# Kernel tuning notes

Hardware: AMD Instinct MI355X
Metric: run time of the kernel (lower is better)

Reference implementation:

```python
import jax, jax.numpy as jnp
import numpy as np

P = 4; PSIZE = 16; EPS = 1e-8; LAM = 1e-3; MF = 2.0; ITERS = 2
BATCH = 64; A = 64; B = 8; C = 16; D = 16; E = 10


def _conv2d(x, w, b, stride, pad):
    y = jax.lax.conv_general_dilated(x, w, (stride, stride), [(pad, pad), (pad, pad)],
                                     dimension_numbers=('NCHW', 'OIHW', 'NCHW'))
    return y + b[None, :, None, None]


def _patches(x, K, stride):
    # x: (b, H, W, F) -> (b, oh, ow, K, K, F) sliding KxK windows with given stride
    b, H, W, F = x.shape
    oh = (H - K) // stride + 1
    ow = (W - K) // stride + 1
    ih = jnp.arange(oh) * stride
    iw = jnp.arange(ow) * stride
    p = x[:, ih[:, None] + jnp.arange(K)[None, :]]          # (b, oh, K, W, F)
    p = p[:, :, :, iw[:, None] + jnp.arange(K)[None, :]]    # (b, oh, K, ow, K, F)
    return p.transpose(0, 1, 3, 2, 4, 5), oh, ow


def _fuzzy_routing(v, a_in, beta_u, beta_a):
    # Fuzzy (c-means style) routing. v: (n, N, Cout, PSIZE) votes, a_in: (n, N).
    n, N, Cc, _ = v.shape
    r = jnp.full((n, N, Cc), 1.0 / Cc, dtype=v.dtype)
    aw = a_in[:, :, None]
    for t in range(ITERS):
        rm = (r ** MF) * aw                                             # fuzzified, activation-weighted
        coeff = rm / (jnp.sum(rm, axis=1, keepdims=True) + EPS)         # (n, N, C)
        mu = jnp.einsum('bnc,bncp->bcp', coeff, v)                      # (n, C, PSIZE)
        if t < ITERS - 1:
            dist = jnp.sum((v - mu[:, None]) ** 2, axis=-1) + EPS       # (n, N, C)
            inv = dist ** (-1.0 / (MF - 1.0))
            r = inv / (jnp.sum(inv, axis=2, keepdims=True) + EPS)
    sigma_sq = jnp.einsum('bnc,bncp->bcp', coeff, (v - mu[:, None]) ** 2) + EPS
    r_sum = jnp.sum((r ** MF) * aw, axis=1)                             # (n, C)
    cost = (beta_u[None, :, None] + 0.5 * jnp.log(sigma_sq)) * r_sum[:, :, None]
    a_out = jax.nn.sigmoid(LAM * (beta_a[None, :] - jnp.sum(cost, axis=2)))
    return mu, a_out


def _conv_caps(pose, a, W, beta_u, beta_a, K, stride):
    # pose: (b, H, W, Bi, PSIZE), a: (b, H, W, Bi); W: (K*K*Bi, Co, P, P)
    b, H, Wd, Bi, _ = pose.shape
    Co = W.shape[1]
    pp, oh, ow = _patches(pose.reshape(b, H, Wd, Bi * PSIZE), K, stride)
    ap, _, _ = _patches(a, K, stride)
    n = b * oh * ow
    pp = pp.reshape(n, K * K * Bi, P, P)
    ap = ap.reshape(n, K * K * Bi)
    v = jnp.einsum('nipq,icqr->nicpr', pp, W).reshape(n, K * K * Bi, Co, PSIZE)
    mu, a_out = _fuzzy_routing(v, ap, beta_u, beta_a)
    return mu.reshape(b, oh, ow, Co, PSIZE), a_out.reshape(b, oh, ow, Co)


def _class_caps(pose, a, W, beta_u, beta_a):
    # K=1, weight-shared over positions, with coordinate addition.
    b, H, Wd, Bi, _ = pose.shape
    Co = W.shape[1]
    v = jnp.einsum('bhwipq,icqr->bhwicpr', pose.reshape(b, H, Wd, Bi, P, P), W)
    v = v.reshape(b, H, Wd, Bi, Co, PSIZE)
    ch = (jnp.arange(H, dtype=v.dtype) / H)[None, :, None, None, None]
    cw = (jnp.arange(Wd, dtype=v.dtype) / Wd)[None, None, :, None, None]
    v = v.at[..., 0].add(ch)
    v = v.at[..., 1].add(cw)
    v = v.reshape(b, H * Wd * Bi, Co, PSIZE)
    return _fuzzy_routing(v, a.reshape(b, -1), beta_u, beta_a)


def setup_inputs():
    key = jax.random.key(0)
    ks = jax.random.split(key, 8)
    return {
        'x': jax.random.normal(ks[0], (BATCH, 1, 32, 32), jnp.float32),
        'conv1_w': jax.random.normal(ks[1], (A, 1, 5, 5), jnp.float32) * 0.1,
        'conv1_b': jnp.zeros((A,), jnp.float32),
        'bn_g': jnp.ones((A,), jnp.float32),
        'bn_b': jnp.zeros((A,), jnp.float32),
        'bn_mean': jnp.zeros((A,), jnp.float32),
        'bn_var': jnp.ones((A,), jnp.float32),
        'prim_pose_w': jax.random.normal(ks[2], (B * PSIZE, A, 1, 1), jnp.float32) * 0.1,
        'prim_pose_b': jnp.zeros((B * PSIZE,), jnp.float32),
        'prim_a_w': jax.random.normal(ks[3], (B, A, 1, 1), jnp.float32) * 0.1,
        'prim_a_b': jnp.zeros((B,), jnp.float32),
        'w1': jax.random.normal(ks[4], (3 * 3 * B, C, P, P), jnp.float32),
        'bu1': jnp.zeros((C,), jnp.float32),
        'ba1': jnp.zeros((C,), jnp.float32),
        'w2': jax.random.normal(ks[5], (3 * 3 * C, D, P, P), jnp.float32),
        'bu2': jnp.zeros((D,), jnp.float32),
        'ba2': jnp.zeros((D,), jnp.float32),
        'wc': jax.random.normal(ks[6], (D, E, P, P), jnp.float32),
        'buc': jnp.zeros((E,), jnp.float32),
        'bac': jnp.zeros((E,), jnp.float32),
    }


def reference(x, conv1_w, conv1_b, bn_g, bn_b, bn_mean, bn_var,
              prim_pose_w, prim_pose_b, prim_a_w, prim_a_b,
              w1, bu1, ba1, w2, bu2, ba2, wc, buc, bac):
    y = _conv2d(x, conv1_w, conv1_b, 2, 2)                               # (b, A, 16, 16)
    inv_std = jax.lax.rsqrt(bn_var + 1e-3)
    y = (y - bn_mean[None, :, None, None]) * (bn_g * inv_std)[None, :, None, None] + bn_b[None, :, None, None]
    y = jax.nn.relu(y)
    pose = _conv2d(y, prim_pose_w, prim_pose_b, 1, 0)                    # (b, B*16, 16, 16)
    a = jax.nn.sigmoid(_conv2d(y, prim_a_w, prim_a_b, 1, 0))             # (b, B, 16, 16)
    b_, _, H, Wd = a.shape
    pose = pose.transpose(0, 2, 3, 1).reshape(b_, H, Wd, B, PSIZE)
    a = a.transpose(0, 2, 3, 1)
    pose1, a1 = _conv_caps(pose, a, w1, bu1, ba1, 3, 2)
    pose2, a2 = _conv_caps(pose1, a1, w2, bu2, ba2, 3, 1)
    _, a_class = _class_caps(pose2, a2, wc, buc, bac)                    # (b, E)
    return a_class
```

## Files before the change

kernel.cpp:

```cpp
#include <hip/hip_runtime.h>
#include <math.h>

#define EPS_ 1e-8f
#define LAM_ 1e-3f

__global__ __launch_bounds__(256) void k_conv_bn(
    const float* __restrict__ x, const float* __restrict__ cw, const float* __restrict__ cb,
    const float* __restrict__ g, const float* __restrict__ bb,
    const float* __restrict__ mean, const float* __restrict__ var,
    float* __restrict__ y)
{
    int t = blockIdx.x * 256 + threadIdx.x;
    int ch = t & 63, w = (t >> 6) & 15, h = (t >> 10) & 15, b = t >> 14;
    const float* xb = x + b * 1024;
    const float* wc = cw + ch * 25;
    float acc = cb[ch];
    #pragma unroll
    for (int kh = 0; kh < 5; ++kh) {
        int ih = h * 2 - 2 + kh;
        if (ih < 0 || ih > 31) continue;
        #pragma unroll
        for (int kw = 0; kw < 5; ++kw) {
            int iw = w * 2 - 2 + kw;
            if (iw < 0 || iw > 31) continue;
            acc = fmaf(xb[ih * 32 + iw], wc[kh * 5 + kw], acc);
        }
    }
    float v = (acc - mean[ch]) * (g[ch] * rsqrtf(var[ch] + 1e-3f)) + bb[ch];
    y[t] = fmaxf(v, 0.f);
}

__global__ __launch_bounds__(256) void k_transw(
    const float* __restrict__ w1, const float* __restrict__ w2, const float* __restrict__ wc,
    const float* __restrict__ pw, const float* __restrict__ pb,
    const float* __restrict__ aw, const float* __restrict__ ab,
    float* __restrict__ w1t, float* __restrict__ w2t, float* __restrict__ wct,
    float* __restrict__ wpt)
{
    int t = blockIdx.x * 256 + threadIdx.x;
    if (t < 3616 * 16) {
        int m = t >> 4, e = t & 15, r = e >> 2, q = e & 3;
        const float* src; float* dst;
        if (m < 1152)      { src = w1 + m * 16;          dst = w1t + m * 16; }
        else if (m < 3456) { src = w2 + (m - 1152) * 16; dst = w2t + (m - 1152) * 16; }
        else               { src = wc + (m - 3456) * 16; dst = wct + (m - 3456) * 16; }
        dst[e] = src[q * 4 + r];
    } else if (t < 3616 * 16 + 65 * 136) {
        int idx = t - 3616 * 16;
        int o = idx % 136, j = idx / 136;
        float v;
        if (j == 64)       v = (o < 128) ? pb[o] : ab[o - 128];
        else if (o < 128)  v = pw[o * 64 + j];
        else               v = aw[(o - 128) * 64 + j];
        wpt[j * 136 + o] = v;
    }
}

__global__ __launch_bounds__(256) void k_prim(
    const float* __restrict__ y, const float* __restrict__ wpt,
    float* __restrict__ poseP, float* __restrict__ aP)
{
    int t = blockIdx.x * 256 + threadIdx.x;
    if (t >= 16384 * 34) return;
    int oq = t % 34;
    int pos = t / 34;
    const float* yp = y + pos * 64;
    float4 acc = *(const float4*)(wpt + 64 * 136 + oq * 4);
    #pragma unroll
    for (int j0 = 0; j0 < 64; j0 += 4) {
        float4 y4 = *(const float4*)(yp + j0);
        float4 w0 = *(const float4*)(wpt + (j0 + 0) * 136 + oq * 4);
        float4 w1 = *(const float4*)(wpt + (j0 + 1) * 136 + oq * 4);
        float4 w2 = *(const float4*)(wpt + (j0 + 2) * 136 + oq * 4);
        float4 w3 = *(const float4*)(wpt + (j0 + 3) * 136 + oq * 4);
        acc.x = fmaf(y4.x, w0.x, fmaf(y4.y, w1.x, fmaf(y4.z, w2.x, fmaf(y4.w, w3.x, acc.x))));
        acc.y = fmaf(y4.x, w0.y, fmaf(y4.y, w1.y, fmaf(y4.z, w2.y, fmaf(y4.w, w3.y, acc.y))));
        acc.z = fmaf(y4.x, w0.z, fmaf(y4.y, w1.z, fmaf(y4.z, w2.z, fmaf(y4.w, w3.z, acc.z))));
        acc.w = fmaf(y4.x, w0.w, fmaf(y4.y, w1.w, fmaf(y4.z, w2.w, fmaf(y4.w, w3.w, acc.w))));
    }
    if (oq < 32) {
        ((float4*)(poseP + pos * 128))[oq] = acc;
    } else {
        int oo = (oq - 32) * 4;
        float* ad = aP + pos * 8 + oo;
        ad[0] = 1.f / (1.f + __expf(-acc.x));
        ad[1] = 1.f / (1.f + __expf(-acc.y));
        ad[2] = 1.f / (1.f + __expf(-acc.z));
        ad[3] = 1.f / (1.f + __expf(-acc.w));
    }
}

template<int N, int C, int K, int S, int H, int W, int Bi, int OH, int OW, int NW>
__global__ __launch_bounds__(NW * 64) void k_caps_split(
    const float* __restrict__ pose_in,
    const float* __restrict__ a_in,
    const float* __restrict__ Wt,
    const float* __restrict__ bu, const float* __restrict__ ba,
    float* __restrict__ pose_out,
    float* __restrict__ a_out)
{
    static_assert(C == 16 && N % (NW * 4) == 0, "");
    constexpr int BLK = NW * 64;
    constexpr int IW  = N / NW;
    constexpr int NIT = IW / 4;

    __shared__ __align__(16) float pp[N * 16];
    __shared__ float ap[N];
    __shared__ __align__(16) float red1[NW][16][20];
    __shared__ __align__(16) float red2[NW][16][20];
    __shared__ float redr[NW][16];

    const int t = threadIdx.x;
    const int w = t >> 6, lane = t & 63;
    const int n_ = blockIdx.x;
    const int b = n_ / (OH * OW);
    const int rem = n_ % (OH * OW);
    const int oh = rem / OW, ow = rem % OW;

    for (int idx = t; idx < N * 4; idx += BLK) {
        int i = idx >> 2, f = idx & 3;
        int bi = i % Bi;
        int k2 = i / Bi;
        int sw = ow * S + (k2 % K), sh = oh * S + (k2 / K);
        const float4* src = (const float4*)(pose_in + (((b * H + sh) * W + sw) * Bi + bi) * 16);
        ((float4*)(pp + i * 16))[f] = src[f];
    }
    for (int i = t; i < N; i += BLK) {
        int bi = i % Bi;
        int k2 = i / Bi;
        int sw = ow * S + (k2 % K), sh = oh * S + (k2 / K);
        ap[i] = a_in[((b * H + sh) * W + sw) * Bi + bi];
    }
    __syncthreads();

    float suma = 0.f;
    for (int i = lane; i < N; i += 64) suma += ap[i];
    #pragma unroll
    for (int m = 1; m < 64; m <<= 1) suma += __shfl_xor(suma, m, 64);
    const float inv0 = __builtin_amdgcn_rcpf(suma + (float)(C * C) * EPS_);

    const int ig = (lane >> 4) & 3, cc = lane & 15;
    const int ibase = w * IW;

    float muU[16];
    #pragma unroll
    for (int e2 = 0; e2 < 16; ++e2) muU[e2] = 0.f;
    #pragma unroll 2
    for (int ii = 0; ii < NIT; ++ii) {
        int i = ibase + ig + ii * 4;
        const float4* pi4 = (const float4*)(pp + i * 16);
        const float4* wt4 = (const float4*)(Wt + (i * C + cc) * 16);
        float4 pv[4] = { pi4[0], pi4[1], pi4[2], pi4[3] };
        float4 wv[4] = { wt4[0], wt4[1], wt4[2], wt4[3] };
        float co = ap[i] * inv0;
        #pragma unroll
        for (int e2 = 0; e2 < 16; ++e2) {
            float4 p4 = pv[e2 >> 2], w4 = wv[e2 & 3];
            float v = p4.x * w4.x + p4.y * w4.y + p4.z * w4.z + p4.w * w4.w;
            muU[e2] = fmaf(co, v, muU[e2]);
        }
    }
    #pragma unroll
    for (int e2 = 0; e2 < 16; ++e2) {
        muU[e2] += __shfl_xor(muU[e2], 16, 64);
        muU[e2] += __shfl_xor(muU[e2], 32, 64);
    }
    if (lane < 16) {
        float4* dst = (float4*)&red1[w][lane][0];
        dst[0] = *(float4*)&muU[0];
        dst[1] = *(float4*)&muU[4];
        dst[2] = *(float4*)&muU[8];
        dst[3] = *(float4*)&muU[12];
    }
    __syncthreads();

    float m0[16];
    {
        #pragma unroll
        for (int f = 0; f < 4; ++f) {
            float4 s = *(const float4*)&red1[0][cc][f * 4];
            #pragma unroll
            for (int ww = 1; ww < NW; ++ww) {
                float4 p = *(const float4*)&red1[ww][cc][f * 4];
                s.x += p.x; s.y += p.y; s.z += p.z; s.w += p.w;
            }
            *(float4*)&m0[f * 4] = s;
        }
    }
    __syncthreads();

    float SvU[16], Sv2U[16];
    #pragma unroll
    for (int e2 = 0; e2 < 16; ++e2) { SvU[e2] = 0.f; Sv2U[e2] = 0.f; }
    float rsum = 0.f;
    #pragma unroll 2
    for (int ii = 0; ii < NIT; ++ii) {
        int i = ibase + ig + ii * 4;
        const float4* pi4 = (const float4*)(pp + i * 16);
        const float4* wt4 = (const float4*)(Wt + (i * C + cc) * 16);
        float4 pv[4] = { pi4[0], pi4[1], pi4[2], pi4[3] };
        float4 wv[4] = { wt4[0], wt4[1], wt4[2], wt4[3] };
        float vv[16];
        float dist = EPS_;
        #pragma unroll
        for (int e2 = 0; e2 < 16; ++e2) {
            float4 p4 = pv[e2 >> 2], w4 = wv[e2 & 3];
            float v = p4.x * w4.x + p4.y * w4.y + p4.z * w4.z + p4.w * w4.w;
            vv[e2] = v;
            float d = v - m0[e2];
            dist = fmaf(d, d, dist);
        }
        float inv = __builtin_amdgcn_rcpf(dist);
        float s = inv;
        #pragma unroll
        for (int m = 1; m < 16; m <<= 1) s += __shfl_xor(s, m, 64);
        float r1 = inv * __builtin_amdgcn_rcpf(s + EPS_);
        float rm = r1 * r1 * ap[i];
        rsum += rm;
        #pragma unroll
        for (int e2 = 0; e2 < 16; ++e2) {
            float rv = rm * vv[e2];
            SvU[e2] += rv;
            Sv2U[e2] = fmaf(rv, vv[e2], Sv2U[e2]);
        }
    }
    #pragma unroll
    for (int e2 = 0; e2 < 16; ++e2) {
        SvU[e2] += __shfl_xor(SvU[e2], 16, 64);
        SvU[e2] += __shfl_xor(SvU[e2], 32, 64);
        Sv2U[e2] += __shfl_xor(Sv2U[e2], 16, 64);
        Sv2U[e2] += __shfl_xor(Sv2U[e2], 32, 64);
    }
    rsum += __shfl_xor(rsum, 16, 64);
    rsum += __shfl_xor(rsum, 32, 64);
    if (lane < 16) {
        float4* d1 = (float4*)&red1[w][lane][0];
        float4* d2 = (float4*)&red2[w][lane][0];
        d1[0] = *(float4*)&SvU[0];  d1[1] = *(float4*)&SvU[4];
        d1[2] = *(float4*)&SvU[8];  d1[3] = *(float4*)&SvU[12];
        d2[0] = *(float4*)&Sv2U[0]; d2[1] = *(float4*)&Sv2U[4];
        d2[2] = *(float4*)&Sv2U[8]; d2[3] = *(float4*)&Sv2U[12];
        redr[w][lane] = rsum;
    }
    __syncthreads();

    if (w == 0) {
        float SvT[16], Sv2T[16];
        #pragma unroll
        for (int f = 0; f < 4; ++f) {
            float4 s1 = *(const float4*)&red1[0][cc][f * 4];
            float4 s2 = *(const float4*)&red2[0][cc][f * 4];
            #pragma unroll
            for (int ww = 1; ww < NW; ++ww) {
                float4 p1 = *(const float4*)&red1[ww][cc][f * 4];
                float4 p2 = *(const float4*)&red2[ww][cc][f * 4];
                s1.x += p1.x; s1.y += p1.y; s1.z += p1.z; s1.w += p1.w;
                s2.x += p2.x; s2.y += p2.y; s2.z += p2.z; s2.w += p2.w;
            }
            *(float4*)&SvT[f * 4] = s1;
            *(float4*)&Sv2T[f * 4] = s2;
        }
        float R = 0.f;
        #pragma unroll
        for (int ww = 0; ww < NW; ++ww) R += redr[ww][cc];

        const float id = 1.f / (R + EPS_);
        const float S0 = R * id;
        const float buc_ = bu[cc];
        float cs = 0.f;
        float4 outv[4];
        #pragma unroll
        for (int e2 = 0; e2 < 16; ++e2) {
            float Sv = SvT[e2] * id;
            float Sv2 = Sv2T[e2] * id;
            float sigma = fmaxf(Sv2 + Sv * Sv * (S0 - 2.f), 0.f) + EPS_;
            cs += (buc_ + 0.5f * __logf(sigma)) * R;
            ((float*)outv)[e2] = Sv;
        }
        if (lane < 16) {
            float4* pd = (float4*)(pose_out + (n_ * C + cc) * 16);
            pd[0] = outv[0]; pd[1] = outv[1]; pd[2] = outv[2]; pd[3] = outv[3];
            a_out[n_ * C + cc] = 1.f / (1.f + __expf(-(LAM_ * (ba[cc] - cs))));
        }
    }
}

template<int N, int C, int H, int W, int Bi, int BLK>
__global__ __launch_bounds__(BLK) void k_caps_class(
    const float* __restrict__ pose_in, const float* __restrict__ a_in,
    const float* __restrict__ Wt,
    const float* __restrict__ bu, const float* __restrict__ ba,
    float* __restrict__ a_out)
{
    constexpr int NW  = BLK / 64;
    constexpr int NIG = BLK / 16;
    constexpr int NIT = (N + NIG - 1) / NIG;

    __shared__ __align__(16) float pp[N * 16];
    __shared__ float ap[N];
    __shared__ float coeff0[N];
    __shared__ float mu0[16 * 17];
    __shared__ float red1[NW * C * 17];
    __shared__ float red2[NW * C * 17];
    __shared__ float redr[NW * C];

    const int t = threadIdx.x;
    const int lane = t & 63;
    const int w = t >> 6;
    const int b = blockIdx.x;

    for (int idx = t; idx < N * 4; idx += BLK) {
        int i = idx >> 2, f = idx & 3;
        int bi = i % Bi;
        int hw = i / Bi;
        int sw = hw % W, sh = hw / W;
        const float4* src = (const float4*)(pose_in + (((b * H + sh) * W + sw) * Bi + bi) * 16);
        ((float4*)(pp + i * 16))[f] = src[f];
    }
    for (int i = t; i < N; i += BLK) {
        int bi = i % Bi;
        int hw = i / Bi;
        int sw = hw % W, sh = hw / W;
        ap[i] = a_in[((b * H + sh) * W + sw) * Bi + bi];
    }
    __syncthreads();

    {
        float part = 0.f;
        for (int i = t; i < N; i += BLK) part += ap[i];
        #pragma unroll
        for (int m = 1; m < 64; m <<= 1) part += __shfl_xor(part, m, 64);
        if (lane == 0) red1[w] = part;
        __syncthreads();
        float s = 0.f;
        #pragma unroll
        for (int ww = 0; ww < NW; ++ww) s += red1[ww];
        float inv0 = __builtin_amdgcn_rcpf(s + (float)(C * C) * EPS_);
        for (int i = t; i < N; i += BLK) coeff0[i] = ap[i] * inv0;
        __syncthreads();
    }

    const int ig = t >> 4, cc = t & 15;

    {
        float muU[16];
        #pragma unroll
        for (int e2 = 0; e2 < 16; ++e2) muU[e2] = 0.f;
        if (cc < C) {
            for (int ii = 0; ii < NIT; ++ii) {
                int i = ig + ii * NIG;
                if (i < N) {
                    const float4* pi4 = (const float4*)(pp + i * 16);
                    const float4* wt4 = (const float4*)(Wt + ((i % Bi) * C + cc) * 16);
                    float4 pv[4] = { pi4[0], pi4[1], pi4[2], pi4[3] };
                    float4 wv[4] = { wt4[0], wt4[1], wt4[2], wt4[3] };
                    float co = coeff0[i];
                    float chv = (float)(i / (W * Bi)) * (1.f / H);
                    float cwv = (float)((i / Bi) % W) * (1.f / W);
                    #pragma unroll
                    for (int e2 = 0; e2 < 16; ++e2) {
                        float4 p4 = pv[e2 >> 2], w4 = wv[e2 & 3];
                        float v = p4.x * w4.x + p4.y * w4.y + p4.z * w4.z + p4.w * w4.w;
                        if (e2 == 0) v += chv;
                        if (e2 == 1) v += cwv;
                        muU[e2] = fmaf(co, v, muU[e2]);
                    }
                }
            }
        }
        #pragma unroll
        for (int e2 = 0; e2 < 16; ++e2) {
            float xv = muU[e2];
            xv += __shfl_xor(xv, 16, 64);
            xv += __shfl_xor(xv, 32, 64);
            if (lane < 16 && lane < C) red1[(w * C + lane) * 17 + e2] = xv;
        }
        __syncthreads();
        if (t < 256) {
            int c = t >> 4, e = t & 15;
            if (c < C) {
                float m = 0.f;
                #pragma unroll
                for (int ww = 0; ww < NW; ++ww) m += red1[(ww * C + c) * 17 + e];
                mu0[c * 17 + e] = m;
            }
        }
        __syncthreads();
    }

    {
        float m0[16];
        if (cc < C) {
            #pragma unroll
            for (int e2 = 0; e2 < 16; ++e2) m0[e2] = mu0[cc * 17 + e2];
        }
        float SvU[16], Sv2U[16];
        #pragma unroll
        for (int e2 = 0; e2 < 16; ++e2) { SvU[e2] = 0.f; Sv2U[e2] = 0.f; }
        float rsumP = 0.f;

        for (int ii = 0; ii < NIT; ++ii) {
            int i = ig + ii * NIG;
            bool act = (i < N);
            float inv = 0.f;
            float vv[16];
            if (act && cc < C) {
                const float4* pi4 = (const float4*)(pp + i * 16);
                const float4* wt4 = (const float4*)(Wt + ((i % Bi) * C + cc) * 16);
                float4 pv[4] = { pi4[0], pi4[1], pi4[2], pi4[3] };
                float4 wv[4] = { wt4[0], wt4[1], wt4[2], wt4[3] };
                float chv = (float)(i / (W * Bi)) * (1.f / H);
                float cwv = (float)((i / Bi) % W) * (1.f / W);
                float dist = EPS_;
                #pragma unroll
                for (int e2 = 0; e2 < 16; ++e2) {
                    float4 p4 = pv[e2 >> 2], w4 = wv[e2 & 3];
                    float v = p4.x * w4.x + p4.y * w4.y + p4.z * w4.z + p4.w * w4.w;
                    if (e2 == 0) v += chv;
                    if (e2 == 1) v += cwv;
                    vv[e2] = v;
                    float d = v - m0[e2];
                    dist = fmaf(d, d, dist);
                }
                inv = __builtin_amdgcn_rcpf(dist);
            }
            float s = inv;
            #pragma unroll
            for (int m = 1; m < 16; m <<= 1) s += __shfl_xor(s, m, 64);
            if (act && cc < C) {
                float r1 = inv * __builtin_amdgcn_rcpf(s + EPS_);
                float rm = r1 * r1 * ap[i];
                rsumP += rm;
                #pragma unroll
                for (int e2 = 0; e2 < 16; ++e2) {
                    SvU[e2] = fmaf(rm, vv[e2], SvU[e2]);
                    Sv2U[e2] = fmaf(rm * vv[e2], vv[e2], Sv2U[e2]);
                }
            }
        }
        #pragma unroll
        for (int e2 = 0; e2 < 16; ++e2) {
            float xv = SvU[e2];
            xv += __shfl_xor(xv, 16, 64);
            xv += __shfl_xor(xv, 32, 64);
            float yv = Sv2U[e2];
            yv += __shfl_xor(yv, 16, 64);
            yv += __shfl_xor(yv, 32, 64);
            if (lane < 16 && lane < C) {
                red1[(w * C + lane) * 17 + e2] = xv;
                red2[(w * C + lane) * 17 + e2] = yv;
            }
        }
        {
            float rv = rsumP;
            rv += __shfl_xor(rv, 16, 64);
            rv += __shfl_xor(rv, 32, 64);
            if (lane < 16 && lane < C) redr[w * C + lane] = rv;
        }
        __syncthreads();
    }

    if (t < 256) {
        int c = t >> 4, e = t & 15;
        if (c < C) {
            float SvT = 0.f, Sv2T = 0.f, R = 0.f;
            #pragma unroll
            for (int ww = 0; ww < NW; ++ww) {
                SvT  += red1[(ww * C + c) * 17 + e];
                Sv2T += red2[(ww * C + c) * 17 + e];
                R    += redr[ww * C + c];
            }
            float id = 1.f / (R + EPS_);
            float S0 = R * id;
            float Sv = SvT * id;
            float Sv2 = Sv2T * id;
            float sigma = fmaxf(Sv2 + Sv * Sv * (S0 - 2.f), 0.f) + EPS_;
            float cost = (bu[c] + 0.5f * __logf(sigma)) * R;
            float cs = cost;
            #pragma unroll
            for (int m = 1; m < 16; m <<= 1) cs += __shfl_xor(cs, m, 64);
            if (e == 0) a_out[b * C + c] = 1.f / (1.f + __expf(-(LAM_ * (ba[c] - cs))));
        }
    }
}

extern "C" void kernel_launch(void* const* d_in, const int* in_sizes, int n_in,
                              void* d_out, int out_size, void* d_ws, size_t ws_size,
                              hipStream_t stream)
{
    const float* x   = (const float*)d_in[0];
    const float* c1w = (const float*)d_in[1];
    const float* c1b = (const float*)d_in[2];
    const float* bng = (const float*)d_in[3];
    const float* bnb = (const float*)d_in[4];
    const float* bnm = (const float*)d_in[5];
    const float* bnv = (const float*)d_in[6];
    const float* ppw = (const float*)d_in[7];
    const float* ppb = (const float*)d_in[8];
    const float* paw = (const float*)d_in[9];
    const float* pab = (const float*)d_in[10];
    const float* w1  = (const float*)d_in[11];
    const float* bu1 = (const float*)d_in[12];
    const float* ba1 = (const float*)d_in[13];
    const float* w2  = (const float*)d_in[14];
    const float* bu2 = (const float*)d_in[15];
    const float* ba2 = (const float*)d_in[16];
    const float* wcp = (const float*)d_in[17];
    const float* buc = (const float*)d_in[18];
    const float* bac = (const float*)d_in[19];
    float* out = (float*)d_out;

    float* ws    = (float*)d_ws;
    float* y     = ws;
    float* poseP = y + 1048576;
    float* aP    = poseP + 2097152;
    float* pose1 = aP + 131072;
    float* a1    = pose1 + 802816;
    float* pose2 = a1 + 50176;
    float* a2    = pose2 + 409600;
    float* w1t   = a2 + 25600;
    float* w2t   = w1t + 18432;
    float* wct   = w2t + 36864;
    float* wpt   = wct + 2560;

    hipLaunchKernelGGL(k_transw, dim3((3616 * 16 + 65 * 136 + 255) / 256), dim3(256), 0, stream,
                       w1, w2, wcp, ppw, ppb, paw, pab, w1t, w2t, wct, wpt);
    hipLaunchKernelGGL(k_conv_bn, dim3(4096), dim3(256), 0, stream,
                       x, c1w, c1b, bng, bnb, bnm, bnv, y);
    hipLaunchKernelGGL(k_prim, dim3((16384 * 34 + 255) / 256), dim3(256), 0, stream,
                       y, wpt, poseP, aP);
    hipLaunchKernelGGL((k_caps_split<72, 16, 3, 2, 16, 16, 8, 7, 7, 2>), dim3(3136), dim3(128), 0, stream,
                       poseP, aP, w1t, bu1, ba1, pose1, a1);
    hipLaunchKernelGGL((k_caps_split<144, 16, 3, 1, 7, 7, 16, 5, 5, 4>), dim3(1600), dim3(256), 0, stream,
                       pose1, a1, w2t, bu2, ba2, pose2, a2);
    hipLaunchKernelGGL((k_caps_class<400, 10, 5, 5, 16, 1024>), dim3(64), dim3(1024), 0, stream,
                       pose2, a2, wct, buc, bac, out);
}
```

Baseline: 263.1 us.

## Process two output positions per block in conv-caps to reuse transform weights

The conv-capsule routing kernel now handles two output capsule positions per block. Each transform-weight float4 load from global memory is shared across both positions' vote computations, halving weight traffic per position. The second layer also drops from four waves to two per block. This doubles live registers for the accumulators (mu, Sv, Sv2 for two positions), which risks lower occupancy or spills, and halves the grid size.

```diff
diff --git a/kernel.cpp b/kernel.cpp
--- a/kernel.cpp
+++ b/kernel.cpp
@@ -91,7 +91,7 @@
 }
 
 template<int N, int C, int K, int S, int H, int W, int Bi, int OH, int OW, int NW>
-__global__ __launch_bounds__(NW * 64) void k_caps_split(
+__global__ __launch_bounds__(NW * 64) void k_caps_split2(
     const float* __restrict__ pose_in,
     const float* __restrict__ a_in,
     const float* __restrict__ Wt,
@@ -99,161 +99,203 @@
     float* __restrict__ pose_out,
     float* __restrict__ a_out)
 {
-    static_assert(C == 16 && N % (NW * 4) == 0, "");
+    static_assert(C == 16 && N % (NW * 4) == 0 && NW >= 2, "");
     constexpr int BLK = NW * 64;
     constexpr int IW  = N / NW;
     constexpr int NIT = IW / 4;
 
-    __shared__ __align__(16) float pp[N * 16];
-    __shared__ float ap[N];
-    __shared__ __align__(16) float red1[NW][16][20];
-    __shared__ __align__(16) float red2[NW][16][20];
-    __shared__ float redr[NW][16];
+    __shared__ __align__(16) float pp[2][N * 16];
+    __shared__ float ap[2][N];
+    __shared__ __align__(16) float red1[NW][2][16][20];
+    __shared__ __align__(16) float red2[NW][2][16][20];
+    __shared__ float redr[NW][2][16];
 
     const int t = threadIdx.x;
     const int w = t >> 6, lane = t & 63;
-    const int n_ = blockIdx.x;
-    const int b = n_ / (OH * OW);
-    const int rem = n_ % (OH * OW);
-    const int oh = rem / OW, ow = rem % OW;
-
-    for (int idx = t; idx < N * 4; idx += BLK) {
-        int i = idx >> 2, f = idx & 3;
+    const int n0 = blockIdx.x * 2;
+
+    int bb_[2], oh_[2], ow_[2];
+    #pragma unroll
+    for (int g = 0; g < 2; ++g) {
+        int n_ = n0 + g;
+        bb_[g] = n_ / (OH * OW);
+        int rem = n_ % (OH * OW);
+        oh_[g] = rem / OW; ow_[g] = rem % OW;
+    }
+
+    for (int idx = t; idx < 2 * N * 4; idx += BLK) {
+        int g = idx / (N * 4);
+        int r2 = idx - g * (N * 4);
+        int i = r2 >> 2, f = r2 & 3;
         int bi = i % Bi;
         int k2 = i / Bi;
-        int sw = ow * S + (k2 % K), sh = oh * S + (k2 / K);
-        const float4* src = (const float4*)(pose_in + (((b * H + sh) * W + sw) * Bi + bi) * 16);
-        ((float4*)(pp + i * 16))[f] = src[f];
-    }
-    for (int i = t; i < N; i += BLK) {
+        int sw = ow_[g] * S + (k2 % K), sh = oh_[g] * S + (k2 / K);
+        const float4* src = (const float4*)(pose_in + (((bb_[g] * H + sh) * W + sw) * Bi + bi) * 16);
+        ((float4*)(pp[g] + i * 16))[f] = src[f];
+    }
+    for (int idx = t; idx < 2 * N; idx += BLK) {
+        int g = idx / N;
+        int i = idx - g * N;
         int bi = i % Bi;
         int k2 = i / Bi;
-        int sw = ow * S + (k2 % K), sh = oh * S + (k2 / K);
-        ap[i] = a_in[((b * H + sh) * W + sw) * Bi + bi];
+        int sw = ow_[g] * S + (k2 % K), sh = oh_[g] * S + (k2 / K);
+        ap[g][i] = a_in[((bb_[g] * H + sh) * W + sw) * Bi + bi];
     }
     __syncthreads();
 
-    float suma = 0.f;
-    for (int i = lane; i < N; i += 64) suma += ap[i];
-    #pragma unroll
-    for (int m = 1; m < 64; m <<= 1) suma += __shfl_xor(suma, m, 64);
-    const float inv0 = __builtin_amdgcn_rcpf(suma + (float)(C * C) * EPS_);
+    float s0A = 0.f, s0B = 0.f;
+    for (int i = lane; i < N; i += 64) { s0A += ap[0][i]; s0B += ap[1][i]; }
+    #pragma unroll
+    for (int m = 1; m < 64; m <<= 1) { s0A += __shfl_xor(s0A, m, 64); s0B += __shfl_xor(s0B, m, 64); }
+    const float inv0A = __builtin_amdgcn_rcpf(s0A + (float)(C * C) * EPS_);
+    const float inv0B = __builtin_amdgcn_rcpf(s0B + (float)(C * C) * EPS_);
 
     const int ig = (lane >> 4) & 3, cc = lane & 15;
     const int ibase = w * IW;
 
-    float muU[16];
-    #pragma unroll
-    for (int e2 = 0; e2 < 16; ++e2) muU[e2] = 0.f;
-    #pragma unroll 2
+    float muA[16], muB[16];
+    #pragma unroll
+    for (int e2 = 0; e2 < 16; ++e2) { muA[e2] = 0.f; muB[e2] = 0.f; }
     for (int ii = 0; ii < NIT; ++ii) {
         int i = ibase + ig + ii * 4;
-        const float4* pi4 = (const float4*)(pp + i * 16);
         const float4* wt4 = (const float4*)(Wt + (i * C + cc) * 16);
-        float4 pv[4] = { pi4[0], pi4[1], pi4[2], pi4[3] };
         float4 wv[4] = { wt4[0], wt4[1], wt4[2], wt4[3] };
-        float co = ap[i] * inv0;
+        const float4* pA4 = (const float4*)(pp[0] + i * 16);
+        const float4* pB4 = (const float4*)(pp[1] + i * 16);
+        float4 pA[4] = { pA4[0], pA4[1], pA4[2], pA4[3] };
+        float4 pB[4] = { pB4[0], pB4[1], pB4[2], pB4[3] };
+        float coA = ap[0][i] * inv0A;
+        float coB = ap[1][i] * inv0B;
         #pragma unroll
         for (int e2 = 0; e2 < 16; ++e2) {
-            float4 p4 = pv[e2 >> 2], w4 = wv[e2 & 3];
-            float v = p4.x * w4.x + p4.y * w4.y + p4.z * w4.z + p4.w * w4.w;
-            muU[e2] = fmaf(co, v, muU[e2]);
+            float4 w4 = wv[e2 & 3];
+            float4 a4 = pA[e2 >> 2];
+            float4 b4 = pB[e2 >> 2];
+            float vA = a4.x * w4.x + a4.y * w4.y + a4.z * w4.z + a4.w * w4.w;
+            float vB = b4.x * w4.x + b4.y * w4.y + b4.z * w4.z + b4.w * w4.w;
+            muA[e2] = fmaf(coA, vA, muA[e2]);
+            muB[e2] = fmaf(coB, vB, muB[e2]);
         }
     }
     #pragma unroll
     for (int e2 = 0; e2 < 16; ++e2) {
-        muU[e2] += __shfl_xor(muU[e2], 16, 64);
-        muU[e2] += __shfl_xor(muU[e2], 32, 64);
+        muA[e2] += __shfl_xor(muA[e2], 16, 64);
+        muA[e2] += __shfl_xor(muA[e2], 32, 64);
+        muB[e2] += __shfl_xor(muB[e2], 16, 64);
+        muB[e2] += __shfl_xor(muB[e2], 32, 64);
     }
     if (lane < 16) {
-        float4* dst = (float4*)&red1[w][lane][0];
-        dst[0] = *(float4*)&muU[0];
-        dst[1] = *(float4*)&muU[4];
-        dst[2] = *(float4*)&muU[8];
-        dst[3] = *(float4*)&muU[12];
+        float4* dA = (float4*)&red1[w][0][lane][0];
+        float4* dB = (float4*)&red1[w][1][lane][0];
+        dA[0] = *(float4*)&muA[0]; dA[1] = *(float4*)&muA[4];
+        dA[2] = *(float4*)&muA[8]; dA[3] = *(float4*)&muA[12];
+        dB[0] = *(float4*)&muB[0]; dB[1] = *(float4*)&muB[4];
+        dB[2] = *(float4*)&muB[8]; dB[3] = *(float4*)&muB[12];
     }
     __syncthreads();
 
-    float m0[16];
-    {
+    float m0A[16], m0B[16];
+    #pragma unroll
+    for (int f = 0; f < 4; ++f) {
+        float4 sA = *(const float4*)&red1[0][0][cc][f * 4];
+        float4 sB = *(const float4*)&red1[0][1][cc][f * 4];
+        #pragma unroll
+        for (int ww = 1; ww < NW; ++ww) {
+            float4 qA = *(const float4*)&red1[ww][0][cc][f * 4];
+            float4 qB = *(const float4*)&red1[ww][1][cc][f * 4];
+            sA.x += qA.x; sA.y += qA.y; sA.z += qA.z; sA.w += qA.w;
+            sB.x += qB.x; sB.y += qB.y; sB.z += qB.z; sB.w += qB.w;
+        }
+        *(float4*)&m0A[f * 4] = sA;
+        *(float4*)&m0B[f * 4] = sB;
+    }
+    __syncthreads();
+
+    float SvA[16], Sv2A[16], SvB[16], Sv2B[16];
+    #pragma unroll
+    for (int e2 = 0; e2 < 16; ++e2) { SvA[e2] = 0.f; Sv2A[e2] = 0.f; SvB[e2] = 0.f; Sv2B[e2] = 0.f; }
+    float rsA = 0.f, rsB = 0.f;
+    for (int ii = 0; ii < NIT; ++ii) {
+        int i = ibase + ig + ii * 4;
+        const float4* wt4 = (const float4*)(Wt + (i * C + cc) * 16);
+        float4 wv[4] = { wt4[0], wt4[1], wt4[2], wt4[3] };
+        const float4* pA4 = (const float4*)(pp[0] + i * 16);
+        const float4* pB4 = (const float4*)(pp[1] + i * 16);
+        float4 pA[4] = { pA4[0], pA4[1], pA4[2], pA4[3] };
+        float4 pB[4] = { pB4[0], pB4[1], pB4[2], pB4[3] };
+        float vvA[16], vvB[16];
+        float dA = EPS_, dB = EPS_;
+        #pragma unroll
+        for (int e2 = 0; e2 < 16; ++e2) {
+            float4 w4 = wv[e2 & 3];
+            float4 a4 = pA[e2 >> 2];
+            float4 b4 = pB[e2 >> 2];
+            float vA = a4.x * w4.x + a4.y * w4.y + a4.z * w4.z + a4.w * w4.w;
+            float vB = b4.x * w4.x + b4.y * w4.y + b4.z * w4.z + b4.w * w4.w;
+            vvA[e2] = vA; vvB[e2] = vB;
+            float eA = vA - m0A[e2];
+            float eB = vB - m0B[e2];
+            dA = fmaf(eA, eA, dA);
+            dB = fmaf(eB, eB, dB);
+        }
+        float invA = __builtin_amdgcn_rcpf(dA);
+        float invB = __builtin_amdgcn_rcpf(dB);
+        float sA = invA, sB = invB;
+        #pragma unroll
+        for (int m = 1; m < 16; m <<= 1) { sA += __shfl_xor(sA, m, 64); sB += __shfl_xor(sB, m, 64); }
+        float r1A = invA * __builtin_amdgcn_rcpf(sA + EPS_);
+        float r1B = invB * __builtin_amdgcn_rcpf(sB + EPS_);
+        float rmA = r1A * r1A * ap[0][i];
+        float rmB = r1B * r1B * ap[1][i];
+        rsA += rmA; rsB += rmB;
+        #pragma unroll
+        for (int e2 = 0; e2 < 16; ++e2) {
+            float rvA = rmA * vvA[e2];
+            float rvB = rmB * vvB[e2];
+            SvA[e2] += rvA;
+            SvB[e2] += rvB;
+            Sv2A[e2] = fmaf(rvA, vvA[e2], Sv2A[e2]);
+            Sv2B[e2] = fmaf(rvB, vvB[e2], Sv2B[e2]);
+        }
+    }
+    #pragma unroll
+    for (int e2 = 0; e2 < 16; ++e2) {
+        SvA[e2] += __shfl_xor(SvA[e2], 16, 64);  SvA[e2] += __shfl_xor(SvA[e2], 32, 64);
+        Sv2A[e2] += __shfl_xor(Sv2A[e2], 16, 64); Sv2A[e2] += __shfl_xor(Sv2A[e2], 32, 64);
+        SvB[e2] += __shfl_xor(SvB[e2], 16, 64);  SvB[e2] += __shfl_xor(SvB[e2], 32, 64);
+        Sv2B[e2] += __shfl_xor(Sv2B[e2], 16, 64); Sv2B[e2] += __shfl_xor(Sv2B[e2], 32, 64);
+    }
+    rsA += __shfl_xor(rsA, 16, 64); rsA += __shfl_xor(rsA, 32, 64);
+    rsB += __shfl_xor(rsB, 16, 64); rsB += __shfl_xor(rsB, 32, 64);
+    if (lane < 16) {
+        float4* d1A = (float4*)&red1[w][0][lane][0];
+        float4* d2A = (float4*)&red2[w][0][lane][0];
+        float4* d1B = (float4*)&red1[w][1][lane][0];
+        float4* d2B = (float4*)&red2[w][1][lane][0];
+        d1A[0] = *(float4*)&SvA[0];  d1A[1] = *(float4*)&SvA[4];
+        d1A[2] = *(float4*)&SvA[8];  d1A[3] = *(float4*)&SvA[12];
+        d2A[0] = *(float4*)&Sv2A[0]; d2A[1] = *(float4*)&Sv2A[4];
+        d2A[2] = *(float4*)&Sv2A[8]; d2A[3] = *(float4*)&Sv2A[12];
+        d1B[0] = *(float4*)&SvB[0];  d1B[1] = *(float4*)&SvB[4];
+        d1B[2] = *(float4*)&SvB[8];  d1B[3] = *(float4*)&SvB[12];
+        d2B[0] = *(float4*)&Sv2B[0]; d2B[1] = *(float4*)&Sv2B[4];
+        d2B[2] = *(float4*)&Sv2B[8]; d2B[3] = *(float4*)&Sv2B[12];
+        redr[w][0][lane] = rsA;
+        redr[w][1][lane] = rsB;
+    }
+    __syncthreads();
+
+    if (w < 2) {
+        const int g = w;
+        float SvT[16], Sv2T[16];
         #pragma unroll
         for (int f = 0; f < 4; ++f) {
-            float4 s = *(const float4*)&red1[0][cc][f * 4];
+            float4 s1 = *(const float4*)&red1[0][g][cc][f * 4];
+            float4 s2 = *(const float4*)&red2[0][g][cc][f * 4];
             #pragma unroll
             for (int ww = 1; ww < NW; ++ww) {
-                float4 p = *(const float4*)&red1[ww][cc][f * 4];
-                s.x += p.x; s.y += p.y; s.z += p.z; s.w += p.w;
-            }
-            *(float4*)&m0[f * 4] = s;
-        }
-    }
-    __syncthreads();
-
-    float SvU[16], Sv2U[16];
-    #pragma unroll
-    for (int e2 = 0; e2 < 16; ++e2) { SvU[e2] = 0.f; Sv2U[e2] = 0.f; }
-    float rsum = 0.f;
-    #pragma unroll 2
-    for (int ii = 0; ii < NIT; ++ii) {
-        int i = ibase + ig + ii * 4;
-        const float4* pi4 = (const float4*)(pp + i * 16);
-        const float4* wt4 = (const float4*)(Wt + (i * C + cc) * 16);
-        float4 pv[4] = { pi4[0], pi4[1], pi4[2], pi4[3] };
-        float4 wv[4] = { wt4[0], wt4[1], wt4[2], wt4[3] };
-        float vv[16];
-        float dist = EPS_;
-        #pragma unroll
-        for (int e2 = 0; e2 < 16; ++e2) {
-            float4 p4 = pv[e2 >> 2], w4 = wv[e2 & 3];
-            float v = p4.x * w4.x + p4.y * w4.y + p4.z * w4.z + p4.w * w4.w;
-            vv[e2] = v;
-            float d = v - m0[e2];
-            dist = fmaf(d, d, dist);
-        }
-        float inv = __builtin_amdgcn_rcpf(dist);
-        float s = inv;
-        #pragma unroll
-        for (int m = 1; m < 16; m <<= 1) s += __shfl_xor(s, m, 64);
-        float r1 = inv * __builtin_amdgcn_rcpf(s + EPS_);
-        float rm = r1 * r1 * ap[i];
-        rsum += rm;
-        #pragma unroll
-        for (int e2 = 0; e2 < 16; ++e2) {
-            float rv = rm * vv[e2];
-            SvU[e2] += rv;
-            Sv2U[e2] = fmaf(rv, vv[e2], Sv2U[e2]);
-        }
-    }
-    #pragma unroll
-    for (int e2 = 0; e2 < 16; ++e2) {
-        SvU[e2] += __shfl_xor(SvU[e2], 16, 64);
-        SvU[e2] += __shfl_xor(SvU[e2], 32, 64);
-        Sv2U[e2] += __shfl_xor(Sv2U[e2], 16, 64);
-        Sv2U[e2] += __shfl_xor(Sv2U[e2], 32, 64);
-    }
-    rsum += __shfl_xor(rsum, 16, 64);
-    rsum += __shfl_xor(rsum, 32, 64);
-    if (lane < 16) {
-        float4* d1 = (float4*)&red1[w][lane][0];
-        float4* d2 = (float4*)&red2[w][lane][0];
-        d1[0] = *(float4*)&SvU[0];  d1[1] = *(float4*)&SvU[4];
-        d1[2] = *(float4*)&SvU[8];  d1[3] = *(float4*)&SvU[12];
-        d2[0] = *(float4*)&Sv2U[0]; d2[1] = *(float4*)&Sv2U[4];
-        d2[2] = *(float4*)&Sv2U[8]; d2[3] = *(float4*)&Sv2U[12];
-        redr[w][lane] = rsum;
-    }
-    __syncthreads();
-
-    if (w == 0) {
-        float SvT[16], Sv2T[16];
-        #pragma unroll
-        for (int f = 0; f < 4; ++f) {
-            float4 s1 = *(const float4*)&red1[0][cc][f * 4];
-            float4 s2 = *(const float4*)&red2[0][cc][f * 4];
-            #pragma unroll
-            for (int ww = 1; ww < NW; ++ww) {
-                float4 p1 = *(const float4*)&red1[ww][cc][f * 4];
-                float4 p2 = *(const float4*)&red2[ww][cc][f * 4];
+                float4 p1 = *(const float4*)&red1[ww][g][cc][f * 4];
+                float4 p2 = *(const float4*)&red2[ww][g][cc][f * 4];
                 s1.x += p1.x; s1.y += p1.y; s1.z += p1.z; s1.w += p1.w;
                 s2.x += p2.x; s2.y += p2.y; s2.z += p2.z; s2.w += p2.w;
             }
@@ -262,7 +304,7 @@
         }
         float R = 0.f;
         #pragma unroll
-        for (int ww = 0; ww < NW; ++ww) R += redr[ww][cc];
+        for (int ww = 0; ww < NW; ++ww) R += redr[ww][g][cc];
 
         const float id = 1.f / (R + EPS_);
         const float S0 = R * id;
@@ -278,6 +320,7 @@
             ((float*)outv)[e2] = Sv;
         }
         if (lane < 16) {
+            int n_ = n0 + g;
             float4* pd = (float4*)(pose_out + (n_ * C + cc) * 16);
             pd[0] = outv[0]; pd[1] = outv[1]; pd[2] = outv[2]; pd[3] = outv[3];
             a_out[n_ * C + cc] = 1.f / (1.f + __expf(-(LAM_ * (ba[cc] - cs))));
@@ -529,9 +572,9 @@
                        x, c1w, c1b, bng, bnb, bnm, bnv, y);
     hipLaunchKernelGGL(k_prim, dim3((16384 * 34 + 255) / 256), dim3(256), 0, stream,
                        y, wpt, poseP, aP);
-    hipLaunchKernelGGL((k_caps_split<72, 16, 3, 2, 16, 16, 8, 7, 7, 2>), dim3(3136), dim3(128), 0, stream,
+    hipLaunchKernelGGL((k_caps_split2<72, 16, 3, 2, 16, 16, 8, 7, 7, 2>), dim3(1568), dim3(128), 0, stream,
                        poseP, aP, w1t, bu1, ba1, pose1, a1);
-    hipLaunchKernelGGL((k_caps_split<144, 16, 3, 1, 7, 7, 16, 5, 5, 4>), dim3(1600), dim3(256), 0, stream,
+    hipLaunchKernelGGL((k_caps_split2<144, 16, 3, 1, 7, 7, 16, 5, 5, 2>), dim3(800), dim3(128), 0, stream,
                        pose1, a1, w2t, bu2, ba2, pose2, a2);
     hipLaunchKernelGGL((k_caps_class<400, 10, 5, 5, 16, 1024>), dim3(64), dim3(1024), 0, stream,
                        pose2, a2, wct, buc, bac, out);
```

Measured after the change: 251.0 us. 4.6% less time.
